# Optimization experiments

Hardware: AMD Instinct MI355X
Metric: run time of the kernel (lower is better)

## Reference

```python
import jax, jax.numpy as jnp
import numpy as np

B, CH, H, W, D = 2, 32, 256, 512, 192


def setup_inputs() -> dict:
    key = jax.random.key(0)
    ks = jax.random.split(key, 10)
    def w(k, shape, fan_in):
        return jax.random.normal(k, shape, jnp.float32) * (1.0 / np.sqrt(fan_in))
    return {
        "x": jax.random.normal(ks[0], (B, CH, H, W), jnp.float32),
        "y": jax.random.normal(ks[1], (B, CH, H, W), jnp.float32),
        # encoder: 1x1 convs ch->64->32->1 (shared for x and y)
        "w1": w(ks[2], (64, CH), CH), "b1": w(ks[3], (64,), CH),
        "w2": w(ks[4], (32, 64), 64), "b2": w(ks[5], (32,), 64),
        "w3": w(ks[6], (1, 32), 32), "b3": w(ks[7], (1,), 32),
        # decoderl: 1x1 conv maxdisp->maxdisp (original code applies decoderl to BOTH volumes)
        "wd": w(ks[8], (D, D), D), "bd": w(ks[9], (D,), D),
    }


def _conv1x1(w, b, h):  # [O,C] x [B,C,H,W] -> [B,O,H,W]
    return jnp.einsum("oc,bchw->bohw", w, h) + b[None, :, None, None]


def _encoder(x, w1, b1, w2, b2, w3, b3):
    h = jax.nn.relu(x)
    h = jax.nn.relu(_conv1x1(w1, b1, h))
    h = jax.nn.relu(_conv1x1(w2, b2, h))
    h = jax.nn.relu(_conv1x1(w3, b3, h))
    return h[:, 0]  # squeeze channel -> [B,H,W]


def _cost_volumes(xf, yf):
    # costx[b,d,h,w] = xf[b,h,w+d] * yf[b,h,w]   (0 where w+d >= W)
    # costy[b,d,h,w] = xf[b,h,w]   * yf[b,h,w-d] (0 where w-d < 0)
    dgrid = jnp.arange(D)
    wgrid = jnp.arange(W)
    x_pad = jnp.pad(xf, ((0, 0), (0, 0), (0, D)))          # zero pad right
    xg = x_pad[:, :, wgrid[None, :] + dgrid[:, None]]       # [B,H,D,W]
    costx = (xg * yf[:, :, None, :]).transpose(0, 2, 1, 3)  # [B,D,H,W]
    y_pad = jnp.pad(yf, ((0, 0), (0, 0), (D, 0)))           # zero pad left
    yg = y_pad[:, :, wgrid[None, :] - dgrid[:, None] + D]   # [B,H,D,W]
    costy = (xf[:, :, None, :] * yg).transpose(0, 2, 1, 3)  # [B,D,H,W]
    return costx, costy


def reference(x, y, w1, b1, w2, b2, w3, b3, wd, bd):
    xf = _encoder(x, w1, b1, w2, b2, w3, b3)
    yf = _encoder(y, w1, b1, w2, b2, w3, b3)
    costx, costy = _cost_volumes(xf, yf)
    probx = jax.nn.softmax(_conv1x1(wd, bd, costx), axis=1)
    proby = jax.nn.softmax(_conv1x1(wd, bd, costy), axis=1)  # decoderl used for both, as in source
    disp_vals = jnp.arange(D, dtype=probx.dtype)
    dispx = jnp.einsum("bdhw,d->bhw", probx, disp_vals)
    dispy = jnp.einsum("bdhw,d->bhw", proby, disp_vals)
    return dispx, dispy
```

## Files before the change

kernel.cpp:

```cpp
#include <hip/hip_runtime.h>


typedef __attribute__((ext_vector_type(8))) __bf16 bf16x8;
typedef __attribute__((ext_vector_type(4))) float  f32x4;
typedef __attribute__((ext_vector_type(4))) int    i32x4;

#define MFMA16x16x32(a,b,c) __builtin_amdgcn_mfma_f32_16x16x32_bf16((a),(b),(c),0,0,0)

constexpr int WW  = 512;
constexpr int HW  = 256 * 512;
constexpr int CHW = 32 * HW;
constexpr int OUTPLANE = 2 * 256 * 512;
constexpr float LOG2E = 1.4426950408889634f;

constexpr int WD_OFF  = 0;
constexpr int WD_SZ   = 192 * 384;
constexpr int CPS     = 1424;
constexpr int XC_OFF  = WD_OFF + WD_SZ;
constexpr int YC_OFF  = XC_OFF + 2 * CPS;
constexpr int BD_OFF  = YC_OFF + 2 * CPS;
constexpr int LDS_BYTES = BD_OFF + 768;

__global__ __launch_bounds__(512)
__attribute__((amdgpu_waves_per_eu(2, 2)))
void panet_fused(const float* __restrict__ gx,  const float* __restrict__ gy,
                 const float* __restrict__ gw1, const float* __restrict__ gb1,
                 const float* __restrict__ gw2, const float* __restrict__ gb2,
                 const float* __restrict__ gw3, const float* __restrict__ gb3,
                 const float* __restrict__ gwd, const float* __restrict__ gbd,
                 float* __restrict__ gout)
{
  extern __shared__ __align__(16) char lds[];
  const int tid  = threadIdx.x;
  const int bh   = blockIdx.x;
  const int b    = bh >> 8;
  const int h    = bh & 255;
  const int lane = tid & 63;
  const int m    = lane & 15;
  const int g    = lane >> 4;
  const int wid  = tid >> 6;

  {
    int* zp = (int*)(lds + XC_OFF);
    for (int i = tid; i < (4 * CPS) / 4; i += 512) zp[i] = 0;

    unsigned short* wds = (unsigned short*)(lds + WD_OFF);
    for (int i = tid; i < 192 * 192; i += 512) {
      const int o = i / 192;
      const int k = i - o * 192;
      const __bf16 v = (__bf16)gwd[i];
      const int byt = o * 384 + ((2 * k) ^ ((o & 7) << 4));
      wds[byt >> 1] = __builtin_bit_cast(unsigned short, v);
    }
    float* bds = (float*)(lds + BD_OFF);
    if (tid < 192) bds[tid] = gbd[tid] * LOG2E;
  }
  __syncthreads();

  {
    bf16x8 A1[4], A2[2][2];
    f32x4  bias1[4], bias2[2], w3v[2];
    #pragma unroll
    for (int Mt = 0; Mt < 4; ++Mt) {
      const float* p = gw1 + (16 * Mt + m) * 32 + 4 * g;
      const f32x4 u0 = *(const f32x4*)p;
      const f32x4 u1 = *(const f32x4*)(p + 16);
      #pragma unroll
      for (int j = 0; j < 4; ++j) { A1[Mt][j] = (__bf16)u0[j]; A1[Mt][j + 4] = (__bf16)u1[j]; }
      bias1[Mt] = *(const f32x4*)(gb1 + 16 * Mt + 4 * g);
    }
    #pragma unroll
    for (int Mt = 0; Mt < 2; ++Mt) {
      #pragma unroll
      for (int s = 0; s < 2; ++s) {
        const float* p = gw2 + (16 * Mt + m) * 64 + 32 * s + 4 * g;
        const f32x4 u0 = *(const f32x4*)p;
        const f32x4 u1 = *(const f32x4*)(p + 16);
        #pragma unroll
        for (int j = 0; j < 4; ++j) { A2[Mt][s][j] = (__bf16)u0[j]; A2[Mt][s][j + 4] = (__bf16)u1[j]; }
      }
      bias2[Mt] = *(const f32x4*)(gb2 + 16 * Mt + 4 * g);
      w3v[Mt]   = *(const f32x4*)(gw3 + 16 * Mt + 4 * g);
    }
    const float b3s = gb3[0];
    const f32x4 zf4 = {0.f, 0.f, 0.f, 0.f};

    for (int u = wid; u < 64; u += 8) {
      const int t  = u >> 5;
      const int w0 = (u & 31) << 4;
      const float* src = (t ? gy : gx) + b * CHW + h * WW + w0 + m;

      bf16x8 B1;
      #pragma unroll
      for (int j = 0; j < 8; ++j) {
        const int c = 16 * (j >> 2) + 4 * g + (j & 3);
        B1[j] = (__bf16)fmaxf(src[c * HW], 0.f);
      }
      f32x4 acc1[4];
      #pragma unroll
      for (int Mt = 0; Mt < 4; ++Mt) acc1[Mt] = MFMA16x16x32(A1[Mt], B1, zf4);

      bf16x8 B2[2];
      #pragma unroll
      for (int s = 0; s < 2; ++s) {
        #pragma unroll
        for (int j = 0; j < 4; ++j) {
          B2[s][j]     = (__bf16)fmaxf(acc1[2 * s][j]     + bias1[2 * s][j],     0.f);
          B2[s][j + 4] = (__bf16)fmaxf(acc1[2 * s + 1][j] + bias1[2 * s + 1][j], 0.f);
        }
      }
      f32x4 acc2[2];
      #pragma unroll
      for (int Mt = 0; Mt < 2; ++Mt)
        acc2[Mt] = MFMA16x16x32(A2[Mt][1], B2[1], MFMA16x16x32(A2[Mt][0], B2[0], zf4));

      float s3 = 0.f;
      #pragma unroll
      for (int Mt = 0; Mt < 2; ++Mt)
        #pragma unroll
        for (int r = 0; r < 4; ++r)
          s3 += w3v[Mt][r] * fmaxf(acc2[Mt][r] + bias2[Mt][r], 0.f);
      s3 += __shfl_xor(s3, 16);
      s3 += __shfl_xor(s3, 32);
      const float val = fmaxf(s3 + b3s, 0.f);

      if (lane < 16) {
        const int px = w0 + m;
        const unsigned short bits = __builtin_bit_cast(unsigned short, (__bf16)val);
        if (t == 0) {
          #pragma unroll
          for (int c = 0; c < 2; ++c) {
            const int e = px - c;
            if (e >= 0) ((unsigned short*)(lds + XC_OFF + c * CPS))[e] = bits;
          }
        } else {
          #pragma unroll
          for (int c = 0; c < 2; ++c) {
            const int e = 511 - px - c;
            if (e >= 0) ((unsigned short*)(lds + YC_OFF + c * CPS))[e] = bits;
          }
        }
      }
    }
  }
  __syncthreads();

  {
    const int dir      = wid >> 2;
    const int colbase  = (wid & 3) << 7;
    const char* Bb     = lds + (dir ? YC_OFF : XC_OFF);
    const char* scB    = lds + (dir ? XC_OFF : YC_OFF);
    float* outp = gout + dir * OUTPLANE + (((b << 8) + h) << 9);
    const int Xm   = (m & 7) << 4;
    const int arow = m * 384;
    const float g4 = 4.0f * (float)g;

    for (int chunk = 0; chunk < 4; ++chunk) {
      const int n0 = colbase + (chunk << 5);
      int   laneB[2];
      float sc[2];
      #pragma unroll
      for (int nt = 0; nt < 2; ++nt) {
        const int wc = n0 + 16 * nt + m;
        const int I0 = dir ? (511 - wc) : wc;
        const int c  = I0 & 1;
        laneB[nt] = c * CPS + 2 * (I0 - c) + 16 * g;
        const int sidx = dir ? wc : (511 - wc);
        sc[nt] = LOG2E * (float)(((const __bf16*)scB)[sidx]);
      }
      bf16x8 bfr[6][2];
      #pragma unroll
      for (int ks = 0; ks < 6; ++ks) {
        #pragma unroll
        for (int nt = 0; nt < 2; ++nt) {
          const int* bp = (const int*)(Bb + laneB[nt] + (ks << 6));
          i32x4 q = { bp[0], bp[1], bp[2], bp[3] };
          bfr[ks][nt] = __builtin_bit_cast(bf16x8, q);
        }
      }

      float mx0 = -3.4e38f, mx1 = -3.4e38f;
      float s0 = 0.f, s1 = 0.f, ws0 = 0.f, ws1 = 0.f;

      #pragma unroll 2
      for (int mp = 0; mp < 6; ++mp) {
        f32x4 a00 = {0,0,0,0}, a01 = {0,0,0,0}, a10 = {0,0,0,0}, a11 = {0,0,0,0};
        #pragma unroll
        for (int ks = 0; ks < 6; ++ks) {
          const int inner = ((ks << 6) + (g << 4)) ^ Xm;
          const char* ap = lds + WD_OFF + (mp * 2) * 6144 + arow + inner;
          const bf16x8 af0 = *(const bf16x8*)(ap);
          const bf16x8 af1 = *(const bf16x8*)(ap + 6144);
          a00 = MFMA16x16x32(af0, bfr[ks][0], a00);
          a01 = MFMA16x16x32(af0, bfr[ks][1], a01);
          a10 = MFMA16x16x32(af1, bfr[ks][0], a10);
          a11 = MFMA16x16x32(af1, bfr[ks][1], a11);
        }
        const f32x4 bd0 = *(const f32x4*)(lds + BD_OFF + (mp * 2) * 64 + 16 * g);
        const f32x4 bd1 = *(const f32x4*)(lds + BD_OFF + (mp * 2 + 1) * 64 + 16 * g);
        const float ob = (float)(32 * mp);

        {
          f32x4 L0, L1;
          #pragma unroll
          for (int r = 0; r < 4; ++r) {
            L0[r] = fmaf(sc[0], a00[r], bd0[r]);
            L1[r] = fmaf(sc[0], a10[r], bd1[r]);
          }
          const float pm = fmaxf(fmaxf(fmaxf(L0[0], L0[1]), fmaxf(L0[2], L0[3])),
                                 fmaxf(fmaxf(L1[0], L1[1]), fmaxf(L1[2], L1[3])));
          const float nm = fmaxf(mx0, pm);
          const float f  = exp2f(mx0 - nm);
          float ls = 0.f, lw = 0.f;
          #pragma unroll
          for (int r = 0; r < 4; ++r) {
            const float p0 = exp2f(L0[r] - nm);
            const float p1 = exp2f(L1[r] - nm);
            ls += p0 + p1;
            lw += (ob + (float)r) * p0 + (ob + 16.f + (float)r) * p1;
          }
          s0  = fmaf(s0,  f, ls);
          ws0 = fmaf(ws0, f, lw);
          mx0 = nm;
        }
        {
          f32x4 L0, L1;
          #pragma unroll
          for (int r = 0; r < 4; ++r) {
            L0[r] = fmaf(sc[1], a01[r], bd0[r]);
            L1[r] = fmaf(sc[1], a11[r], bd1[r]);
          }
          const float pm = fmaxf(fmaxf(fmaxf(L0[0], L0[1]), fmaxf(L0[2], L0[3])),
                                 fmaxf(fmaxf(L1[0], L1[1]), fmaxf(L1[2], L1[3])));
          const float nm = fmaxf(mx1, pm);
          const float f  = exp2f(mx1 - nm);
          float ls = 0.f, lw = 0.f;
          #pragma unroll
          for (int r = 0; r < 4; ++r) {
            const float p0 = exp2f(L0[r] - nm);
            const float p1 = exp2f(L1[r] - nm);
            ls += p0 + p1;
            lw += (ob + (float)r) * p0 + (ob + 16.f + (float)r) * p1;
          }
          s1  = fmaf(s1,  f, ls);
          ws1 = fmaf(ws1, f, lw);
          mx1 = nm;
        }
      }

      #pragma unroll
      for (int nt = 0; nt < 2; ++nt) {
        const float mx = nt ? mx1 : mx0;
        const float s  = nt ? s1  : s0;
        const float ws = nt ? ws1 : ws0;
        float M = fmaxf(mx, __shfl_xor(mx, 16));
        M = fmaxf(M, __shfl_xor(M, 32));
        const float f = exp2f(mx - M);
        float sr = s * f;
        float wr = (ws + g4 * s) * f;
        sr += __shfl_xor(sr, 16); sr += __shfl_xor(sr, 32);
        wr += __shfl_xor(wr, 16); wr += __shfl_xor(wr, 32);
        if (lane < 16) outp[n0 + 16 * nt + m] = wr / sr;
      }
    }
  }
}

extern "C" void kernel_launch(void* const* d_in, const int* in_sizes, int n_in,
                              void* d_out, int out_size, void* d_ws, size_t ws_size,
                              hipStream_t stream) {
  const float* x  = (const float*)d_in[0];
  const float* y  = (const float*)d_in[1];
  const float* w1 = (const float*)d_in[2];
  const float* b1 = (const float*)d_in[3];
  const float* w2 = (const float*)d_in[4];
  const float* b2 = (const float*)d_in[5];
  const float* w3 = (const float*)d_in[6];
  const float* b3 = (const float*)d_in[7];
  const float* wd = (const float*)d_in[8];
  const float* bd = (const float*)d_in[9];

  (void)hipFuncSetAttribute((const void*)panet_fused,
                            hipFuncAttributeMaxDynamicSharedMemorySize, LDS_BYTES);
  panet_fused<<<512, 512, LDS_BYTES, stream>>>(x, y, w1, b1, w2, b2, w3, b3, wd, bd,
                                               (float*)d_out);
}
```

Measured before the change: 100.2 us.

## Split fused kernel into encoder and correlation kernels with halved LDS weight tiles

Splits the single fused kernel into two launches. The first encodes x and y rows into a bf16 workspace and pre-swizzles the decoder weights and bias. The second computes the cost-volume decoder softmax with one block per row and direction, loading half of the decoder weights into LDS at a time and merging the two online-softmax partial results. This is meant to cut LDS use per block and double the block count, which should raise occupancy and parallelism. The cost is an extra launch, a global round trip for the features, repeated weight loads from the workspace, and 8 staggered copies of the shifted feature row so B-fragment loads stay aligned.

```diff
diff --git a/kernel.cpp b/kernel.cpp
--- a/kernel.cpp
+++ b/kernel.cpp
@@ -3,192 +3,210 @@
 
 typedef __attribute__((ext_vector_type(8))) __bf16 bf16x8;
 typedef __attribute__((ext_vector_type(4))) float  f32x4;
-typedef __attribute__((ext_vector_type(4))) int    i32x4;
 
 #define MFMA16x16x32(a,b,c) __builtin_amdgcn_mfma_f32_16x16x32_bf16((a),(b),(c),0,0,0)
 
 constexpr int WW  = 512;
 constexpr int HW  = 256 * 512;
 constexpr int CHW = 32 * HW;
-constexpr int OUTPLANE = 2 * 256 * 512;
 constexpr float LOG2E = 1.4426950408889634f;
 
-constexpr int WD_OFF  = 0;
-constexpr int WD_SZ   = 192 * 384;
-constexpr int CPS     = 1424;
-constexpr int XC_OFF  = WD_OFF + WD_SZ;
-constexpr int YC_OFF  = XC_OFF + 2 * CPS;
-constexpr int BD_OFF  = YC_OFF + 2 * CPS;
-constexpr int LDS_BYTES = BD_OFF + 768;
+constexpr size_t XFB_OFF = 0;
+constexpr size_t WDP_OFF = 2 * 262144 * 2;
+constexpr size_t BDP_OFF = WDP_OFF + 73728;
 
 __global__ __launch_bounds__(512)
-__attribute__((amdgpu_waves_per_eu(2, 2)))
-void panet_fused(const float* __restrict__ gx,  const float* __restrict__ gy,
-                 const float* __restrict__ gw1, const float* __restrict__ gb1,
-                 const float* __restrict__ gw2, const float* __restrict__ gb2,
-                 const float* __restrict__ gw3, const float* __restrict__ gb3,
-                 const float* __restrict__ gwd, const float* __restrict__ gbd,
-                 float* __restrict__ gout)
+void panet_encode(const float* __restrict__ gx,  const float* __restrict__ gy,
+                  const float* __restrict__ gw1, const float* __restrict__ gb1,
+                  const float* __restrict__ gw2, const float* __restrict__ gb2,
+                  const float* __restrict__ gw3, const float* __restrict__ gb3,
+                  const float* __restrict__ gwd, const float* __restrict__ gbd,
+                  char* __restrict__ ws)
 {
-  extern __shared__ __align__(16) char lds[];
-  const int tid  = threadIdx.x;
-  const int bh   = blockIdx.x;
-  const int b    = bh >> 8;
-  const int h    = bh & 255;
+  const int blk = blockIdx.x;
+  const int tid = threadIdx.x;
+
+  if (blk >= 1024) {
+    const int pi = blk - 1024;
+    unsigned short* wdp = (unsigned short*)(ws + WDP_OFF);
+    for (int idx = tid; idx < 12 * 192; idx += 512) {
+      const int oo = idx / 192;
+      const int k  = idx - oo * 192;
+      const int o  = 12 * pi + oo;
+      const int half = (o >= 96) ? 1 : 0;
+      const int op = o - 96 * half;
+      const __bf16 v = (__bf16)gwd[o * 192 + k];
+      const int byt = half * 36864 + op * 384 + ((2 * k) ^ ((op & 7) << 4));
+      wdp[byt >> 1] = __builtin_bit_cast(unsigned short, v);
+    }
+    if (pi == 0) {
+      float* bdp = (float*)(ws + BDP_OFF);
+      if (tid < 192) bdp[tid] = gbd[tid] * LOG2E;
+    }
+    return;
+  }
+
+  const int t    = blk >> 9;
+  const int bh   = blk & 511;
   const int lane = tid & 63;
   const int m    = lane & 15;
   const int g    = lane >> 4;
   const int wid  = tid >> 6;
 
-  {
-    int* zp = (int*)(lds + XC_OFF);
-    for (int i = tid; i < (4 * CPS) / 4; i += 512) zp[i] = 0;
-
-    unsigned short* wds = (unsigned short*)(lds + WD_OFF);
-    for (int i = tid; i < 192 * 192; i += 512) {
-      const int o = i / 192;
-      const int k = i - o * 192;
-      const __bf16 v = (__bf16)gwd[i];
-      const int byt = o * 384 + ((2 * k) ^ ((o & 7) << 4));
-      wds[byt >> 1] = __builtin_bit_cast(unsigned short, v);
-    }
-    float* bds = (float*)(lds + BD_OFF);
-    if (tid < 192) bds[tid] = gbd[tid] * LOG2E;
-  }
-  __syncthreads();
-
-  {
-    bf16x8 A1[4], A2[2][2];
-    f32x4  bias1[4], bias2[2], w3v[2];
-    #pragma unroll
-    for (int Mt = 0; Mt < 4; ++Mt) {
-      const float* p = gw1 + (16 * Mt + m) * 32 + 4 * g;
+  bf16x8 A1[4], A2[2][2];
+  f32x4  bias1[4], bias2[2], w3v[2];
+  #pragma unroll
+  for (int Mt = 0; Mt < 4; ++Mt) {
+    const float* p = gw1 + (16 * Mt + m) * 32 + 4 * g;
+    const f32x4 u0 = *(const f32x4*)p;
+    const f32x4 u1 = *(const f32x4*)(p + 16);
+    #pragma unroll
+    for (int j = 0; j < 4; ++j) { A1[Mt][j] = (__bf16)u0[j]; A1[Mt][j + 4] = (__bf16)u1[j]; }
+    bias1[Mt] = *(const f32x4*)(gb1 + 16 * Mt + 4 * g);
+  }
+  #pragma unroll
+  for (int Mt = 0; Mt < 2; ++Mt) {
+    #pragma unroll
+    for (int s = 0; s < 2; ++s) {
+      const float* p = gw2 + (16 * Mt + m) * 64 + 32 * s + 4 * g;
       const f32x4 u0 = *(const f32x4*)p;
       const f32x4 u1 = *(const f32x4*)(p + 16);
       #pragma unroll
-      for (int j = 0; j < 4; ++j) { A1[Mt][j] = (__bf16)u0[j]; A1[Mt][j + 4] = (__bf16)u1[j]; }
-      bias1[Mt] = *(const f32x4*)(gb1 + 16 * Mt + 4 * g);
-    }
-    #pragma unroll
-    for (int Mt = 0; Mt < 2; ++Mt) {
-      #pragma unroll
-      for (int s = 0; s < 2; ++s) {
-        const float* p = gw2 + (16 * Mt + m) * 64 + 32 * s + 4 * g;
-        const f32x4 u0 = *(const f32x4*)p;
-        const f32x4 u1 = *(const f32x4*)(p + 16);
-        #pragma unroll
-        for (int j = 0; j < 4; ++j) { A2[Mt][s][j] = (__bf16)u0[j]; A2[Mt][s][j + 4] = (__bf16)u1[j]; }
-      }
-      bias2[Mt] = *(const f32x4*)(gb2 + 16 * Mt + 4 * g);
-      w3v[Mt]   = *(const f32x4*)(gw3 + 16 * Mt + 4 * g);
-    }
-    const float b3s = gb3[0];
-    const f32x4 zf4 = {0.f, 0.f, 0.f, 0.f};
-
-    for (int u = wid; u < 64; u += 8) {
-      const int t  = u >> 5;
-      const int w0 = (u & 31) << 4;
-      const float* src = (t ? gy : gx) + b * CHW + h * WW + w0 + m;
-
-      bf16x8 B1;
-      #pragma unroll
-      for (int j = 0; j < 8; ++j) {
-        const int c = 16 * (j >> 2) + 4 * g + (j & 3);
-        B1[j] = (__bf16)fmaxf(src[c * HW], 0.f);
-      }
-      f32x4 acc1[4];
-      #pragma unroll
-      for (int Mt = 0; Mt < 4; ++Mt) acc1[Mt] = MFMA16x16x32(A1[Mt], B1, zf4);
-
-      bf16x8 B2[2];
-      #pragma unroll
-      for (int s = 0; s < 2; ++s) {
-        #pragma unroll
-        for (int j = 0; j < 4; ++j) {
-          B2[s][j]     = (__bf16)fmaxf(acc1[2 * s][j]     + bias1[2 * s][j],     0.f);
-          B2[s][j + 4] = (__bf16)fmaxf(acc1[2 * s + 1][j] + bias1[2 * s + 1][j], 0.f);
-        }
-      }
-      f32x4 acc2[2];
-      #pragma unroll
-      for (int Mt = 0; Mt < 2; ++Mt)
-        acc2[Mt] = MFMA16x16x32(A2[Mt][1], B2[1], MFMA16x16x32(A2[Mt][0], B2[0], zf4));
-
-      float s3 = 0.f;
-      #pragma unroll
-      for (int Mt = 0; Mt < 2; ++Mt)
-        #pragma unroll
-        for (int r = 0; r < 4; ++r)
-          s3 += w3v[Mt][r] * fmaxf(acc2[Mt][r] + bias2[Mt][r], 0.f);
-      s3 += __shfl_xor(s3, 16);
-      s3 += __shfl_xor(s3, 32);
-      const float val = fmaxf(s3 + b3s, 0.f);
-
-      if (lane < 16) {
-        const int px = w0 + m;
-        const unsigned short bits = __builtin_bit_cast(unsigned short, (__bf16)val);
-        if (t == 0) {
-          #pragma unroll
-          for (int c = 0; c < 2; ++c) {
-            const int e = px - c;
-            if (e >= 0) ((unsigned short*)(lds + XC_OFF + c * CPS))[e] = bits;
-          }
-        } else {
-          #pragma unroll
-          for (int c = 0; c < 2; ++c) {
-            const int e = 511 - px - c;
-            if (e >= 0) ((unsigned short*)(lds + YC_OFF + c * CPS))[e] = bits;
-          }
-        }
-      }
-    }
+      for (int j = 0; j < 4; ++j) { A2[Mt][s][j] = (__bf16)u0[j]; A2[Mt][s][j + 4] = (__bf16)u1[j]; }
+    }
+    bias2[Mt] = *(const f32x4*)(gb2 + 16 * Mt + 4 * g);
+    w3v[Mt]   = *(const f32x4*)(gw3 + 16 * Mt + 4 * g);
+  }
+  const float b3s = gb3[0];
+  const f32x4 zf4 = {0.f, 0.f, 0.f, 0.f};
+  const float* base = (t ? gy : gx) + (bh >> 8) * CHW + (bh & 255) * WW;
+  unsigned short* xfb = (unsigned short*)(ws + XFB_OFF) + t * 262144 + bh * 512;
+
+  for (int u = wid; u < 32; u += 8) {
+    const int w0 = u << 4;
+    const float* src = base + w0 + m;
+
+    bf16x8 B1;
+    #pragma unroll
+    for (int j = 0; j < 8; ++j) {
+      const int c = 16 * (j >> 2) + 4 * g + (j & 3);
+      B1[j] = (__bf16)fmaxf(src[c * HW], 0.f);
+    }
+    f32x4 acc1[4];
+    #pragma unroll
+    for (int Mt = 0; Mt < 4; ++Mt) acc1[Mt] = MFMA16x16x32(A1[Mt], B1, zf4);
+
+    bf16x8 B2[2];
+    #pragma unroll
+    for (int s = 0; s < 2; ++s) {
+      #pragma unroll
+      for (int j = 0; j < 4; ++j) {
+        B2[s][j]     = (__bf16)fmaxf(acc1[2 * s][j]     + bias1[2 * s][j],     0.f);
+        B2[s][j + 4] = (__bf16)fmaxf(acc1[2 * s + 1][j] + bias1[2 * s + 1][j], 0.f);
+      }
+    }
+    f32x4 acc2[2];
+    #pragma unroll
+    for (int Mt = 0; Mt < 2; ++Mt)
+      acc2[Mt] = MFMA16x16x32(A2[Mt][1], B2[1], MFMA16x16x32(A2[Mt][0], B2[0], zf4));
+
+    float s3 = 0.f;
+    #pragma unroll
+    for (int Mt = 0; Mt < 2; ++Mt)
+      #pragma unroll
+      for (int r = 0; r < 4; ++r)
+        s3 += w3v[Mt][r] * fmaxf(acc2[Mt][r] + bias2[Mt][r], 0.f);
+    s3 += __shfl_xor(s3, 16);
+    s3 += __shfl_xor(s3, 32);
+    const float val = fmaxf(s3 + b3s, 0.f);
+
+    if (lane < 16)
+      xfb[w0 + m] = __builtin_bit_cast(unsigned short, (__bf16)val);
+  }
+}
+
+constexpr int CPS    = 1424;
+constexpr int K2_WD  = 0;
+constexpr int K2_HK  = 36864;
+constexpr int K2_BD  = K2_HK + 11392;
+constexpr int K2_LDS = K2_BD + 768;
+
+__global__ __launch_bounds__(512)
+void panet_corr(const char* __restrict__ ws, float* __restrict__ gout)
+{
+  __shared__ __align__(16) char lds[K2_LDS];
+  const int blk  = blockIdx.x;
+  const int dir  = blk >> 9;
+  const int bh   = blk & 511;
+  const int tid  = threadIdx.x;
+  const int lane = tid & 63;
+  const int m    = lane & 15;
+  const int g    = lane >> 4;
+  const int wid  = tid >> 6;
+
+  const unsigned short* xfb = (const unsigned short*)(ws + XFB_OFF);
+  const unsigned short* hs = xfb + (dir ? 262144 : 0) + bh * 512;
+  const unsigned short* ss = xfb + (dir ? 0 : 262144) + bh * 512;
+
+  {
+    const f32x4* src = (const f32x4*)(ws + WDP_OFF);
+    f32x4* dst = (f32x4*)(lds + K2_WD);
+    for (int i = tid; i < 36864 / 16; i += 512) dst[i] = src[i];
+    int* zp = (int*)(lds + K2_HK);
+    for (int i = tid; i < 11392 / 4; i += 512) zp[i] = 0;
+    const float* bdp = (const float*)(ws + BDP_OFF);
+    if (tid < 192) ((float*)(lds + K2_BD))[tid] = bdp[tid];
   }
   __syncthreads();
-
-  {
-    const int dir      = wid >> 2;
-    const int colbase  = (wid & 3) << 7;
-    const char* Bb     = lds + (dir ? YC_OFF : XC_OFF);
-    const char* scB    = lds + (dir ? XC_OFF : YC_OFF);
-    float* outp = gout + dir * OUTPLANE + (((b << 8) + h) << 9);
-    const int Xm   = (m & 7) << 4;
-    const int arow = m * 384;
-    const float g4 = 4.0f * (float)g;
-
-    for (int chunk = 0; chunk < 4; ++chunk) {
-      const int n0 = colbase + (chunk << 5);
-      int   laneB[2];
-      float sc[2];
+  #pragma unroll
+  for (int c = 0; c < 8; ++c) {
+    const int e = tid;
+    if (e + c <= 511) {
+      ((unsigned short*)(lds + K2_HK + c * CPS))[e] = hs[dir ? (511 - e - c) : (e + c)];
+    }
+  }
+  __syncthreads();
+
+  const int Xm   = (m & 7) << 4;
+  const int arow = m * 384;
+  const float g4 = 4.0f * (float)g;
+  float stM[2][2], stS[2][2], stW[2][2];
+
+  for (int half = 0; half < 2; ++half) {
+    if (half) {
+      __syncthreads();
+      const f32x4* src = (const f32x4*)(ws + WDP_OFF + 36864);
+      f32x4* dst = (f32x4*)(lds + K2_WD);
+      for (int i = tid; i < 36864 / 16; i += 512) dst[i] = src[i];
+      __syncthreads();
+    }
+    for (int ch = 0; ch < 2; ++ch) {
+      int laneB[2]; float sc[2];
       #pragma unroll
       for (int nt = 0; nt < 2; ++nt) {
-        const int wc = n0 + 16 * nt + m;
-        const int I0 = dir ? (511 - wc) : wc;
-        const int c  = I0 & 1;
+        const int col = wid * 64 + ch * 32 + nt * 16 + m;
+        const int I0  = dir ? (511 - col) : col;
+        const int c   = I0 & 7;
         laneB[nt] = c * CPS + 2 * (I0 - c) + 16 * g;
-        const int sidx = dir ? wc : (511 - wc);
-        sc[nt] = LOG2E * (float)(((const __bf16*)scB)[sidx]);
+        sc[nt] = LOG2E * __builtin_bit_cast(float, (unsigned)ss[col] << 16);
       }
       bf16x8 bfr[6][2];
       #pragma unroll
       for (int ks = 0; ks < 6; ++ks) {
-        #pragma unroll
-        for (int nt = 0; nt < 2; ++nt) {
-          const int* bp = (const int*)(Bb + laneB[nt] + (ks << 6));
-          i32x4 q = { bp[0], bp[1], bp[2], bp[3] };
-          bfr[ks][nt] = __builtin_bit_cast(bf16x8, q);
-        }
+        bfr[ks][0] = *(const bf16x8*)(lds + K2_HK + laneB[0] + (ks << 6));
+        bfr[ks][1] = *(const bf16x8*)(lds + K2_HK + laneB[1] + (ks << 6));
       }
 
       float mx0 = -3.4e38f, mx1 = -3.4e38f;
       float s0 = 0.f, s1 = 0.f, ws0 = 0.f, ws1 = 0.f;
 
-      #pragma unroll 2
-      for (int mp = 0; mp < 6; ++mp) {
+      #pragma unroll 1
+      for (int mp = 0; mp < 3; ++mp) {
         f32x4 a00 = {0,0,0,0}, a01 = {0,0,0,0}, a10 = {0,0,0,0}, a11 = {0,0,0,0};
         #pragma unroll
         for (int ks = 0; ks < 6; ++ks) {
           const int inner = ((ks << 6) + (g << 4)) ^ Xm;
-          const char* ap = lds + WD_OFF + (mp * 2) * 6144 + arow + inner;
+          const char* ap = lds + K2_WD + (mp * 2) * 6144 + arow + inner;
           const bf16x8 af0 = *(const bf16x8*)(ap);
           const bf16x8 af1 = *(const bf16x8*)(ap + 6144);
           a00 = MFMA16x16x32(af0, bfr[ks][0], a00);
@@ -196,9 +214,10 @@
           a10 = MFMA16x16x32(af1, bfr[ks][0], a10);
           a11 = MFMA16x16x32(af1, bfr[ks][1], a11);
         }
-        const f32x4 bd0 = *(const f32x4*)(lds + BD_OFF + (mp * 2) * 64 + 16 * g);
-        const f32x4 bd1 = *(const f32x4*)(lds + BD_OFF + (mp * 2 + 1) * 64 + 16 * g);
-        const float ob = (float)(32 * mp);
+        const int tbase = 6 * half + 2 * mp;
+        const f32x4 bd0 = *(const f32x4*)(lds + K2_BD + tbase * 64 + 16 * g);
+        const f32x4 bd1 = *(const f32x4*)(lds + K2_BD + (tbase + 1) * 64 + 16 * g);
+        const float ob = (float)(96 * half + 32 * mp);
 
         {
           f32x4 L0, L1;
@@ -219,9 +238,7 @@
             ls += p0 + p1;
             lw += (ob + (float)r) * p0 + (ob + 16.f + (float)r) * p1;
           }
-          s0  = fmaf(s0,  f, ls);
-          ws0 = fmaf(ws0, f, lw);
-          mx0 = nm;
+          s0 = fmaf(s0, f, ls);  ws0 = fmaf(ws0, f, lw);  mx0 = nm;
         }
         {
           f32x4 L0, L1;
@@ -242,9 +259,7 @@
             ls += p0 + p1;
             lw += (ob + (float)r) * p0 + (ob + 16.f + (float)r) * p1;
           }
-          s1  = fmaf(s1,  f, ls);
-          ws1 = fmaf(ws1, f, lw);
-          mx1 = nm;
+          s1 = fmaf(s1, f, ls);  ws1 = fmaf(ws1, f, lw);  mx1 = nm;
         }
       }
 
@@ -252,18 +267,35 @@
       for (int nt = 0; nt < 2; ++nt) {
         const float mx = nt ? mx1 : mx0;
         const float s  = nt ? s1  : s0;
-        const float ws = nt ? ws1 : ws0;
+        const float w  = nt ? ws1 : ws0;
         float M = fmaxf(mx, __shfl_xor(mx, 16));
         M = fmaxf(M, __shfl_xor(M, 32));
         const float f = exp2f(mx - M);
         float sr = s * f;
-        float wr = (ws + g4 * s) * f;
+        float wr = (w + g4 * s) * f;
         sr += __shfl_xor(sr, 16); sr += __shfl_xor(sr, 32);
         wr += __shfl_xor(wr, 16); wr += __shfl_xor(wr, 32);
-        if (lane < 16) outp[n0 + 16 * nt + m] = wr / sr;
-      }
-    }
-  }
+        if (half == 0) {
+          stM[ch][nt] = M;  stS[ch][nt] = sr;  stW[ch][nt] = wr;
+        } else {
+          const float MM = fmaxf(stM[ch][nt], M);
+          const float f0 = exp2f(stM[ch][nt] - MM);
+          const float f1 = exp2f(M - MM);
+          stS[ch][nt] = stS[ch][nt] * f0 + sr * f1;
+          stW[ch][nt] = stW[ch][nt] * f0 + wr * f1;
+          stM[ch][nt] = MM;
+        }
+      }
+    }
+  }
+
+  float* outp = gout + dir * 262144 + bh * 512;
+  #pragma unroll
+  for (int ch = 0; ch < 2; ++ch)
+    #pragma unroll
+    for (int nt = 0; nt < 2; ++nt)
+      if (lane < 16)
+        outp[wid * 64 + ch * 32 + nt * 16 + m] = stW[ch][nt] / stS[ch][nt];
 }
 
 extern "C" void kernel_launch(void* const* d_in, const int* in_sizes, int n_in,
@@ -279,9 +311,8 @@
   const float* b3 = (const float*)d_in[7];
   const float* wd = (const float*)d_in[8];
   const float* bd = (const float*)d_in[9];
-
-  (void)hipFuncSetAttribute((const void*)panet_fused,
-                            hipFuncAttributeMaxDynamicSharedMemorySize, LDS_BYTES);
-  panet_fused<<<512, 512, LDS_BYTES, stream>>>(x, y, w1, b1, w2, b2, w3, b3, wd, bd,
-                                               (float*)d_out);
+  char* ws = (char*)d_ws;
+
+  panet_encode<<<1040, 512, 0, stream>>>(x, y, w1, b1, w2, b2, w3, b3, wd, bd, ws);
+  panet_corr<<<1024, 512, 0, stream>>>(ws, (float*)d_out);
 }
```

Result: faster. 94.46 us (-5.8%).
